# Kernel tuning notes

Measured on AMD Instinct MI355X. Metric: run time of the kernel, lower is better.

Reference implementation:

```python
import jax, jax.numpy as jnp
import numpy as np

EPS = 1e-6

def _log_g(x):
    # log of continuous g(x) = where(x>=0, x+0.5, sigmoid(x)) from minGRU paper
    return jnp.where(x >= 0, jnp.log(jax.nn.relu(x) + 0.5), -jax.nn.softplus(-x))

def setup_inputs() -> dict:
    key = jax.random.key(0)
    ks = jax.random.split(key, 4)
    B, S, D, E = 4, 2048, 1024, 8
    scale = D ** -0.5
    return {
        "inputs": jax.random.normal(ks[0], (B, S, D), dtype=jnp.float32),
        "norm_weight": jnp.ones((D,), jnp.float32),
        "router_w": jax.random.normal(ks[1], (E, D), jnp.float32) * scale,
        "router_b": jnp.zeros((E,), jnp.float32),
        "w_hg": jax.random.normal(ks[2], (E, 2 * D, D), jnp.float32) * scale,
        "w_out": jax.random.normal(ks[3], (E, D, D), jnp.float32) * scale,
    }

def reference(inputs, norm_weight, router_w, router_b, w_hg, w_out):
    D = inputs.shape[-1]
    # --- RMSNorm ---
    x = inputs * jax.lax.rsqrt(jnp.mean(inputs * inputs, axis=-1, keepdims=True) + EPS) * norm_weight
    # --- SMEAR: per-sample soft merge of expert weights via mean-pooled routing ---
    probs = jax.nn.softmax(jnp.mean(x, axis=1) @ router_w.T + router_b, axis=-1)  # [B,E]
    W_hg = jnp.einsum('be,ekd->bkd', probs, w_hg)    # [B,2D,D] merged to_hidden_and_gate
    W_out = jnp.einsum('be,eod->bod', probs, w_out)  # [B,D,D]  merged to_out
    # --- minGRU with merged weights (log-space parallel scan, no initial state) ---
    hg = jnp.einsum('bsd,bkd->bsk', x, W_hg)         # [B,S,2D]
    hidden, gate = hg[..., :D], hg[..., D:]
    log_coeffs = -jax.nn.softplus(gate)                      # log(1 - z_t)
    log_values = -jax.nn.softplus(-gate) + _log_g(hidden)    # log z_t + log g(h~_t)
    a_star = jnp.cumsum(log_coeffs, axis=1)
    log_h = a_star + jax.lax.cumlogsumexp(log_values - a_star, axis=1)
    h = jnp.exp(log_h)                               # [B,S,D] recurrent states
    new_state = h[:, -1:]                            # [B,1,D]
    out = jnp.einsum('bsk,bok->bso', h, W_out)       # proj_out
    aux_loss = jnp.zeros((), inputs.dtype)
    return (out + inputs, new_state, aux_loss)
```

## Files before the change

kernel.cpp:

```cpp
#include <hip/hip_runtime.h>
#include <hip/hip_bf16.h>

#define B_  4
#define S_  2048
#define D_  1024
#define E_  8
#define K2_ 2048

#define CHUNKS 32
#define CLEN   64

typedef __attribute__((ext_vector_type(8))) short short8;
typedef __attribute__((ext_vector_type(4))) float floatx4;

__device__ __forceinline__ void gld16(const void* g, const void* l) {
    __builtin_amdgcn_global_load_lds(
        (const __attribute__((address_space(1))) unsigned int*)g,
        (__attribute__((address_space(3))) unsigned int*)l, 16, 0, 0);
}

__global__ void rmsnorm_k(const float* __restrict__ in, const float* __restrict__ nw,
                          __hip_bfloat16* __restrict__ x) {
    int b = blockIdx.y, s = blockIdx.x, t = threadIdx.x;
    const float* row = in + ((size_t)b * S_ + s) * D_;
    float v[4]; float ss = 0.0f;
#pragma unroll
    for (int i = 0; i < 4; i++) { v[i] = row[t + 256 * i]; ss += v[i] * v[i]; }
#pragma unroll
    for (int o = 32; o > 0; o >>= 1) ss += __shfl_down(ss, o, 64);
    __shared__ float ls[4];
    if ((t & 63) == 0) ls[t >> 6] = ss;
    __syncthreads();
    float tot = ls[0] + ls[1] + ls[2] + ls[3];
    float rs = rsqrtf(tot * (1.0f / (float)D_) + 1e-6f);
    __hip_bfloat16* xr = x + ((size_t)b * S_ + s) * D_;
#pragma unroll
    for (int i = 0; i < 4; i++)
        xr[t + 256 * i] = __float2bfloat16(v[i] * rs * nw[t + 256 * i]);
}

__global__ void xsum_k(const __hip_bfloat16* __restrict__ x, float* __restrict__ xs) {
    int d = blockIdx.x * 256 + threadIdx.x;
    int b = blockIdx.y;
    int s0 = blockIdx.z * 128;
    const __hip_bfloat16* p = x + ((size_t)b * S_ + s0) * D_ + d;
    float acc = 0.0f;
#pragma unroll 4
    for (int s = 0; s < 128; s++) { acc += __bfloat162float(*p); p += D_; }
    atomicAdd(&xs[b * D_ + d], acc);
}

__global__ void router_k(const float* __restrict__ xs, const float* __restrict__ rw,
                         const float* __restrict__ rb, float* __restrict__ probs) {
    int t = threadIdx.x;
    int pair = t >> 3, sub = t & 7;
    int b = pair >> 3, e = pair & 7;
    float acc = 0.0f;
    for (int d = sub; d < D_; d += 8) acc += xs[b * D_ + d] * rw[e * D_ + d];
#pragma unroll
    for (int o = 4; o > 0; o >>= 1) acc += __shfl_down(acc, o, 8);
    __shared__ float lg[32];
    if (sub == 0) lg[pair] = acc * (1.0f / (float)S_) + rb[e];
    __syncthreads();
    if (t < 4) {
        float m = -1e30f;
        for (int e2 = 0; e2 < 8; e2++) m = fmaxf(m, lg[t * 8 + e2]);
        float ssum = 0.0f; float ex[8];
        for (int e2 = 0; e2 < 8; e2++) { ex[e2] = expf(lg[t * 8 + e2] - m); ssum += ex[e2]; }
        for (int e2 = 0; e2 < 8; e2++) probs[t * 8 + e2] = ex[e2] / ssum;
    }
}

__global__ void mix_k(const float* __restrict__ probs, const float* __restrict__ whg_e,
                      const float* __restrict__ wout_e, __hip_bfloat16* __restrict__ Whg,
                      __hip_bfloat16* __restrict__ Wout) {
    __shared__ float P[32];
    int t = threadIdx.x;
    if (t < 32) P[t] = probs[t];
    __syncthreads();
    size_t i = (size_t)blockIdx.x * 256 + t;
    const size_t T1 = (size_t)K2_ * D_;
    const size_t T2 = (size_t)D_ * D_;
    if (i < T1) {
        float a0 = 0, a1 = 0, a2 = 0, a3 = 0;
#pragma unroll
        for (int e = 0; e < 8; e++) {
            float w = whg_e[(size_t)e * T1 + i];
            a0 += P[0 * 8 + e] * w; a1 += P[1 * 8 + e] * w;
            a2 += P[2 * 8 + e] * w; a3 += P[3 * 8 + e] * w;
        }
        Whg[0 * T1 + i] = __float2bfloat16(a0); Whg[1 * T1 + i] = __float2bfloat16(a1);
        Whg[2 * T1 + i] = __float2bfloat16(a2); Whg[3 * T1 + i] = __float2bfloat16(a3);
    } else {
        size_t j = i - T1;
        float a0 = 0, a1 = 0, a2 = 0, a3 = 0;
#pragma unroll
        for (int e = 0; e < 8; e++) {
            float w = wout_e[(size_t)e * T2 + j];
            a0 += P[0 * 8 + e] * w; a1 += P[1 * 8 + e] * w;
            a2 += P[2 * 8 + e] * w; a3 += P[3 * 8 + e] * w;
        }
        Wout[0 * T2 + j] = __float2bfloat16(a0); Wout[1 * T2 + j] = __float2bfloat16(a1);
        Wout[2 * T2 + j] = __float2bfloat16(a2); Wout[3 * T2 + j] = __float2bfloat16(a3);
    }
}

__global__ __launch_bounds__(256) void gemm_hg_cv(
    const __hip_bfloat16* __restrict__ A, const __hip_bfloat16* __restrict__ Bm,
    float* __restrict__ cv) {
    const int K = D_;
    int bz = blockIdx.z;
    A  += (size_t)bz * S_ * D_;
    Bm += (size_t)bz * K2_ * D_;
    float2* CV = (float2*)cv + (size_t)bz * S_ * D_;
    int m0 = blockIdx.y * 128, n0 = blockIdx.x * 64;
    __shared__ __hip_bfloat16 lA[128][64];
    __shared__ __hip_bfloat16 lBh[64][64];
    __shared__ __hip_bfloat16 lBg[64][64];
    int t = threadIdx.x;
    int w = t >> 6, lane = t & 63;
    int lm = lane & 15, quad = lane >> 4;
    int wr = w >> 1, wc = w & 1;
    floatx4 acch[4][2] = {};
    floatx4 accg[4][2] = {};
    int srow = lane >> 3;
    int scolb = (lane & 7) * 16;
    const __hip_bfloat16* Bh = Bm;
    const __hip_bfloat16* Bg = Bm + (size_t)D_ * K;

    for (int k0 = 0; k0 < K; k0 += 64) {
#pragma unroll
        for (int it = 0; it < 4; it++) {
            int r0 = (w * 4 + it) * 8;
            gld16((const char*)(A + (size_t)(m0 + r0 + srow) * K + k0) + scolb,
                  &lA[r0][0]);
        }
#pragma unroll
        for (int it = 0; it < 2; it++) {
            int r0 = (w * 2 + it) * 8;
            gld16((const char*)(Bh + (size_t)(n0 + r0 + srow) * K + k0) + scolb,
                  &lBh[r0][0]);
            gld16((const char*)(Bg + (size_t)(n0 + r0 + srow) * K + k0) + scolb,
                  &lBg[r0][0]);
        }
        __syncthreads();
#pragma unroll
        for (int kk = 0; kk < 64; kk += 32) {
            short8 af[4], bh[2], bg[2];
#pragma unroll
            for (int i = 0; i < 4; i++)
                af[i] = *(const short8*)(&lA[wr * 64 + i * 16 + lm][kk + quad * 8]);
#pragma unroll
            for (int j = 0; j < 2; j++) {
                bh[j] = *(const short8*)(&lBh[wc * 32 + j * 16 + lm][kk + quad * 8]);
                bg[j] = *(const short8*)(&lBg[wc * 32 + j * 16 + lm][kk + quad * 8]);
            }
#pragma unroll
            for (int i = 0; i < 4; i++)
#pragma unroll
                for (int j = 0; j < 2; j++) {
                    acch[i][j] = __builtin_amdgcn_mfma_f32_16x16x32_bf16(
                        af[i], bh[j], acch[i][j], 0, 0, 0);
                    accg[i][j] = __builtin_amdgcn_mfma_f32_16x16x32_bf16(
                        af[i], bg[j], accg[i][j], 0, 0, 0);
                }
        }
        __syncthreads();
    }
#pragma unroll
    for (int i = 0; i < 4; i++) {
#pragma unroll
        for (int j = 0; j < 2; j++) {
#pragma unroll
            for (int r = 0; r < 4; r++) {
                int m = m0 + wr * 64 + i * 16 + quad * 4 + r;
                int n = n0 + wc * 32 + j * 16 + lm;
                float hid = acch[i][j][r];
                float g   = accg[i][j][r];
                float c  = 1.0f / (1.0f + expf(g));
                float sg = 1.0f / (1.0f + expf(-g));
                float gfn = (hid >= 0.0f) ? (hid + 0.5f)
                                          : (1.0f / (1.0f + expf(-hid)));
                CV[(size_t)m * D_ + n] = make_float2(c, sg * gfn);
            }
        }
    }
}

#define TM 128
#define TN 128
#define TBK 64
__global__ __launch_bounds__(256) void gemm_bf16_bt(
    const __hip_bfloat16* __restrict__ A, const __hip_bfloat16* __restrict__ Bm,
    float* __restrict__ C, const float* __restrict__ R,
    int M, int N, int K, size_t sa, size_t sb, size_t sc, size_t sr) {
    int bz = blockIdx.z;
    A += (size_t)bz * sa; Bm += (size_t)bz * sb; C += (size_t)bz * sc;
    if (R) R += (size_t)bz * sr;
    int m0 = blockIdx.y * TM, n0 = blockIdx.x * TN;
    __shared__ __hip_bfloat16 lA[TM][TBK];
    __shared__ __hip_bfloat16 lB[TN][TBK];
    int t = threadIdx.x;
    int w = t >> 6, lane = t & 63;
    int lm = lane & 15, quad = lane >> 4;
    int wr = w >> 1, wc = w & 1;
    floatx4 acc[4][4] = {};
    int srow = lane >> 3;
    int scolb = (lane & 7) * 16;

    for (int k0 = 0; k0 < K; k0 += TBK) {
#pragma unroll
        for (int it = 0; it < 4; it++) {
            int r0 = (w * 4 + it) * 8;
            gld16((const char*)(A + (size_t)(m0 + r0 + srow) * K + k0) + scolb,
                  &lA[r0][0]);
            gld16((const char*)(Bm + (size_t)(n0 + r0 + srow) * K + k0) + scolb,
                  &lB[r0][0]);
        }
        __syncthreads();
#pragma unroll
        for (int kk = 0; kk < TBK; kk += 32) {
            short8 af[4], bf[4];
#pragma unroll
            for (int i = 0; i < 4; i++)
                af[i] = *(const short8*)(&lA[wr * 64 + i * 16 + lm][kk + quad * 8]);
#pragma unroll
            for (int j = 0; j < 4; j++)
                bf[j] = *(const short8*)(&lB[wc * 64 + j * 16 + lm][kk + quad * 8]);
#pragma unroll
            for (int i = 0; i < 4; i++)
#pragma unroll
                for (int j = 0; j < 4; j++)
                    acc[i][j] = __builtin_amdgcn_mfma_f32_16x16x32_bf16(
                        af[i], bf[j], acc[i][j], 0, 0, 0);
        }
        __syncthreads();
    }
#pragma unroll
    for (int i = 0; i < 4; i++) {
#pragma unroll
        for (int j = 0; j < 4; j++) {
#pragma unroll
            for (int r = 0; r < 4; r++) {
                int m = m0 + wr * 64 + i * 16 + quad * 4 + r;
                int n = n0 + wc * 64 + j * 16 + lm;
                float v = acc[i][j][r];
                if (R) v += R[(size_t)m * N + n];
                C[(size_t)m * N + n] = v;
            }
        }
    }
}

__global__ void scanA_k(const float* __restrict__ cv, float* __restrict__ Cc,
                        float* __restrict__ Vc) {
    int b = blockIdx.z, c = blockIdx.y;
    int d = blockIdx.x * 256 + threadIdx.x;
    const float2* p = (const float2*)cv + ((size_t)b * S_ + c * CLEN) * D_ + d;
    float P = 1.0f, V = 0.0f;
    for (int s = 0; s < CLEN; s++) {
        float2 e = *p;
        P *= e.x;
        V = e.x * V + e.y;
        p += D_;
    }
    size_t idx = ((size_t)(b * CHUNKS + c)) * D_ + d;
    Cc[idx] = P; Vc[idx] = V;
}

__global__ void scanB_k(const float* __restrict__ Cc, const float* __restrict__ Vc,
                        float* __restrict__ Hi) {
    int b = blockIdx.y;
    int d = blockIdx.x * 256 + threadIdx.x;
    float h = 0.0f;
    for (int c = 0; c < CHUNKS; c++) {
        size_t idx = ((size_t)(b * CHUNKS + c)) * D_ + d;
        Hi[idx] = h;
        h = Cc[idx] * h + Vc[idx];
    }
}

__global__ void scanC_k(const float* __restrict__ cv, const float* __restrict__ Hi,
                        __hip_bfloat16* __restrict__ hout, float* __restrict__ ns) {
    int b = blockIdx.z, c = blockIdx.y;
    int d = blockIdx.x * 256 + threadIdx.x;
    const float2* p = (const float2*)cv + ((size_t)b * S_ + c * CLEN) * D_ + d;
    float h = Hi[((size_t)(b * CHUNKS + c)) * D_ + d];
    for (int s = 0; s < CLEN; s++) {
        float2 e = *p;
        h = e.x * h + e.y;
        hout[((size_t)b * S_ + c * CLEN + s) * D_ + d] = __float2bfloat16(h);
        if (c * CLEN + s == S_ - 1) ns[b * D_ + d] = h;
        p += D_;
    }
}

__global__ void aux_k(float* o) { if (threadIdx.x == 0) o[0] = 0.0f; }

extern "C" void kernel_launch(void* const* d_in, const int* in_sizes, int n_in,
                              void* d_out_v, int out_size, void* d_ws, size_t ws_size,
                              hipStream_t stream) {
    const float* inputs = (const float*)d_in[0];
    const float* nw     = (const float*)d_in[1];
    const float* rw     = (const float*)d_in[2];
    const float* rb     = (const float*)d_in[3];
    const float* whg_e  = (const float*)d_in[4];
    const float* wout_e = (const float*)d_in[5];
    float* out = (float*)d_out_v;

    float* ws = (float*)d_ws;
    float*          cv      = ws;
    __hip_bfloat16* x_bf    = (__hip_bfloat16*)(ws + 16777216);
    __hip_bfloat16* h_bf    = (__hip_bfloat16*)(ws + 20971520);
    __hip_bfloat16* Whg_bf  = (__hip_bfloat16*)(ws + 25165824);
    __hip_bfloat16* Wout_bf = (__hip_bfloat16*)(ws + 29360128);
    float* xsum  = ws + 31457280;
    float* probs = ws + 31461376;
    float* Cc    = ws + 31461408;
    float* Vc    = ws + 31592480;
    float* Hi    = ws + 31723552;

    hipMemsetAsync(xsum, 0, (size_t)B_ * D_ * sizeof(float), stream);

    rmsnorm_k<<<dim3(S_, B_), 256, 0, stream>>>(inputs, nw, x_bf);
    xsum_k<<<dim3(D_ / 256, B_, 16), 256, 0, stream>>>(x_bf, xsum);
    router_k<<<1, 256, 0, stream>>>(xsum, rw, rb, probs);
    mix_k<<<12288, 256, 0, stream>>>(probs, whg_e, wout_e, Whg_bf, Wout_bf);

    gemm_hg_cv<<<dim3(D_ / 64, S_ / 128, B_), 256, 0, stream>>>(x_bf, Whg_bf, cv);

    scanA_k<<<dim3(D_ / 256, CHUNKS, B_), 256, 0, stream>>>(cv, Cc, Vc);
    scanB_k<<<dim3(D_ / 256, B_), 256, 0, stream>>>(Cc, Vc, Hi);
    scanC_k<<<dim3(D_ / 256, CHUNKS, B_), 256, 0, stream>>>(
        cv, Hi, h_bf, out + (size_t)B_ * S_ * D_);

    gemm_bf16_bt<<<dim3(D_ / TN, S_ / TM, B_), 256, 0, stream>>>(
        h_bf, Wout_bf, out, inputs, S_, D_, D_,
        (size_t)S_ * D_, (size_t)D_ * D_, (size_t)S_ * D_, (size_t)S_ * D_);

    aux_k<<<1, 64, 0, stream>>>(out + (size_t)B_ * S_ * D_ + (size_t)B_ * D_);
}
```

Measured before the change: 358.5 us.

## Swizzle GEMM LDS tiles, vectorize scan kernels, fold aux write into router

Both bf16 GEMMs now XOR-swizzle the 16-byte columns of their LDS tiles, both when loading from global memory and when reading MFMA fragments, to avoid LDS bank conflicts. The chunked scan kernels each handle two channels per thread with float4 loads and bfloat162 stores. The chunk count is doubled and chunk length halved for more parallelism, and scratch offsets are enlarged to fit. The separate aux-loss kernel launch is removed and its zero store moved into the router kernel, saving one launch at the cost of a serial scanB that is twice as long.

Result: faster. 345.9 us (-3.5%).

```diff
diff --git a/kernel.cpp b/kernel.cpp
--- a/kernel.cpp
+++ b/kernel.cpp
@@ -7,8 +7,8 @@
 #define E_  8
 #define K2_ 2048
 
-#define CHUNKS 32
-#define CLEN   64
+#define CHUNKS 64
+#define CLEN   32
 
 typedef __attribute__((ext_vector_type(8))) short short8;
 typedef __attribute__((ext_vector_type(4))) float floatx4;
@@ -51,8 +51,10 @@
 }
 
 __global__ void router_k(const float* __restrict__ xs, const float* __restrict__ rw,
-                         const float* __restrict__ rb, float* __restrict__ probs) {
+                         const float* __restrict__ rb, float* __restrict__ probs,
+                         float* __restrict__ aux) {
     int t = threadIdx.x;
+    if (t == 255) *aux = 0.0f;
     int pair = t >> 3, sub = t & 7;
     int b = pair >> 3, e = pair & 7;
     float acc = 0.0f;
@@ -124,7 +126,7 @@
     floatx4 acch[4][2] = {};
     floatx4 accg[4][2] = {};
     int srow = lane >> 3;
-    int scolb = (lane & 7) * 16;
+    int swzb = ((lane & 7) ^ srow) * 16;
     const __hip_bfloat16* Bh = Bm;
     const __hip_bfloat16* Bg = Bm + (size_t)D_ * K;
 
@@ -132,15 +134,15 @@
 #pragma unroll
         for (int it = 0; it < 4; it++) {
             int r0 = (w * 4 + it) * 8;
-            gld16((const char*)(A + (size_t)(m0 + r0 + srow) * K + k0) + scolb,
+            gld16((const char*)(A + (size_t)(m0 + r0 + srow) * K + k0) + swzb,
                   &lA[r0][0]);
         }
 #pragma unroll
         for (int it = 0; it < 2; it++) {
             int r0 = (w * 2 + it) * 8;
-            gld16((const char*)(Bh + (size_t)(n0 + r0 + srow) * K + k0) + scolb,
+            gld16((const char*)(Bh + (size_t)(n0 + r0 + srow) * K + k0) + swzb,
                   &lBh[r0][0]);
-            gld16((const char*)(Bg + (size_t)(n0 + r0 + srow) * K + k0) + scolb,
+            gld16((const char*)(Bg + (size_t)(n0 + r0 + srow) * K + k0) + swzb,
                   &lBg[r0][0]);
         }
         __syncthreads();
@@ -148,12 +150,15 @@
         for (int kk = 0; kk < 64; kk += 32) {
             short8 af[4], bh[2], bg[2];
 #pragma unroll
-            for (int i = 0; i < 4; i++)
-                af[i] = *(const short8*)(&lA[wr * 64 + i * 16 + lm][kk + quad * 8]);
+            for (int i = 0; i < 4; i++) {
+                int p = (((kk >> 3) + quad) ^ (lm & 7)) * 8;
+                af[i] = *(const short8*)(&lA[wr * 64 + i * 16 + lm][p]);
+            }
 #pragma unroll
             for (int j = 0; j < 2; j++) {
-                bh[j] = *(const short8*)(&lBh[wc * 32 + j * 16 + lm][kk + quad * 8]);
-                bg[j] = *(const short8*)(&lBg[wc * 32 + j * 16 + lm][kk + quad * 8]);
+                int p = (((kk >> 3) + quad) ^ (lm & 7)) * 8;
+                bh[j] = *(const short8*)(&lBh[wc * 32 + j * 16 + lm][p]);
+                bg[j] = *(const short8*)(&lBg[wc * 32 + j * 16 + lm][p]);
             }
 #pragma unroll
             for (int i = 0; i < 4; i++)
@@ -206,15 +211,15 @@
     int wr = w >> 1, wc = w & 1;
     floatx4 acc[4][4] = {};
     int srow = lane >> 3;
-    int scolb = (lane & 7) * 16;
+    int swzb = ((lane & 7) ^ srow) * 16;
 
     for (int k0 = 0; k0 < K; k0 += TBK) {
 #pragma unroll
         for (int it = 0; it < 4; it++) {
             int r0 = (w * 4 + it) * 8;
-            gld16((const char*)(A + (size_t)(m0 + r0 + srow) * K + k0) + scolb,
+            gld16((const char*)(A + (size_t)(m0 + r0 + srow) * K + k0) + swzb,
                   &lA[r0][0]);
-            gld16((const char*)(Bm + (size_t)(n0 + r0 + srow) * K + k0) + scolb,
+            gld16((const char*)(Bm + (size_t)(n0 + r0 + srow) * K + k0) + swzb,
                   &lB[r0][0]);
         }
         __syncthreads();
@@ -222,11 +227,15 @@
         for (int kk = 0; kk < TBK; kk += 32) {
             short8 af[4], bf[4];
 #pragma unroll
-            for (int i = 0; i < 4; i++)
-                af[i] = *(const short8*)(&lA[wr * 64 + i * 16 + lm][kk + quad * 8]);
-#pragma unroll
-            for (int j = 0; j < 4; j++)
-                bf[j] = *(const short8*)(&lB[wc * 64 + j * 16 + lm][kk + quad * 8]);
+            for (int i = 0; i < 4; i++) {
+                int p = (((kk >> 3) + quad) ^ (lm & 7)) * 8;
+                af[i] = *(const short8*)(&lA[wr * 64 + i * 16 + lm][p]);
+            }
+#pragma unroll
+            for (int j = 0; j < 4; j++) {
+                int p = (((kk >> 3) + quad) ^ (lm & 7)) * 8;
+                bf[j] = *(const short8*)(&lB[wc * 64 + j * 16 + lm][p]);
+            }
 #pragma unroll
             for (int i = 0; i < 4; i++)
 #pragma unroll
@@ -255,17 +264,17 @@
 __global__ void scanA_k(const float* __restrict__ cv, float* __restrict__ Cc,
                         float* __restrict__ Vc) {
     int b = blockIdx.z, c = blockIdx.y;
-    int d = blockIdx.x * 256 + threadIdx.x;
-    const float2* p = (const float2*)cv + ((size_t)b * S_ + c * CLEN) * D_ + d;
-    float P = 1.0f, V = 0.0f;
+    int d2 = blockIdx.x * 256 + threadIdx.x;
+    const float4* p = (const float4*)cv + (size_t)(b * S_ + c * CLEN) * (D_ / 2) + d2;
+    float P0 = 1.0f, V0 = 0.0f, P1 = 1.0f, V1 = 0.0f;
+#pragma unroll 4
     for (int s = 0; s < CLEN; s++) {
-        float2 e = *p;
-        P *= e.x;
-        V = e.x * V + e.y;
-        p += D_;
-    }
-    size_t idx = ((size_t)(b * CHUNKS + c)) * D_ + d;
-    Cc[idx] = P; Vc[idx] = V;
+        float4 e = p[(size_t)s * (D_ / 2)];
+        P0 *= e.x; V0 = e.x * V0 + e.y;
+        P1 *= e.z; V1 = e.z * V1 + e.w;
+    }
+    size_t idx = ((size_t)(b * CHUNKS + c)) * D_ + 2 * d2;
+    Cc[idx] = P0; Vc[idx] = V0; Cc[idx + 1] = P1; Vc[idx + 1] = V1;
 }
 
 __global__ void scanB_k(const float* __restrict__ Cc, const float* __restrict__ Vc,
@@ -281,21 +290,23 @@
 }
 
 __global__ void scanC_k(const float* __restrict__ cv, const float* __restrict__ Hi,
-                        __hip_bfloat16* __restrict__ hout, float* __restrict__ ns) {
+                        __hip_bfloat162* __restrict__ hout, float* __restrict__ ns) {
     int b = blockIdx.z, c = blockIdx.y;
-    int d = blockIdx.x * 256 + threadIdx.x;
-    const float2* p = (const float2*)cv + ((size_t)b * S_ + c * CLEN) * D_ + d;
-    float h = Hi[((size_t)(b * CHUNKS + c)) * D_ + d];
+    int d2 = blockIdx.x * 256 + threadIdx.x;
+    const float4* p = (const float4*)cv + (size_t)(b * S_ + c * CLEN) * (D_ / 2) + d2;
+    size_t hidx = ((size_t)(b * CHUNKS + c)) * D_ + 2 * d2;
+    float h0 = Hi[hidx], h1 = Hi[hidx + 1];
+#pragma unroll 4
     for (int s = 0; s < CLEN; s++) {
-        float2 e = *p;
-        h = e.x * h + e.y;
-        hout[((size_t)b * S_ + c * CLEN + s) * D_ + d] = __float2bfloat16(h);
-        if (c * CLEN + s == S_ - 1) ns[b * D_ + d] = h;
-        p += D_;
-    }
-}
-
-__global__ void aux_k(float* o) { if (threadIdx.x == 0) o[0] = 0.0f; }
+        float4 e = p[(size_t)s * (D_ / 2)];
+        h0 = e.x * h0 + e.y;
+        h1 = e.z * h1 + e.w;
+        __hip_bfloat162 hh;
+        hh.x = __float2bfloat16(h0); hh.y = __float2bfloat16(h1);
+        hout[(size_t)(b * S_ + c * CLEN + s) * (D_ / 2) + d2] = hh;
+    }
+    if (c == CHUNKS - 1) { ns[b * D_ + 2 * d2] = h0; ns[b * D_ + 2 * d2 + 1] = h1; }
+}
 
 extern "C" void kernel_launch(void* const* d_in, const int* in_sizes, int n_in,
                               void* d_out_v, int out_size, void* d_ws, size_t ws_size,
@@ -317,26 +328,25 @@
     float* xsum  = ws + 31457280;
     float* probs = ws + 31461376;
     float* Cc    = ws + 31461408;
-    float* Vc    = ws + 31592480;
-    float* Hi    = ws + 31723552;
+    float* Vc    = ws + 31723552;
+    float* Hi    = ws + 31985696;
 
     hipMemsetAsync(xsum, 0, (size_t)B_ * D_ * sizeof(float), stream);
 
     rmsnorm_k<<<dim3(S_, B_), 256, 0, stream>>>(inputs, nw, x_bf);
     xsum_k<<<dim3(D_ / 256, B_, 16), 256, 0, stream>>>(x_bf, xsum);
-    router_k<<<1, 256, 0, stream>>>(xsum, rw, rb, probs);
+    router_k<<<1, 256, 0, stream>>>(xsum, rw, rb, probs,
+                                    out + (size_t)B_ * S_ * D_ + (size_t)B_ * D_);
     mix_k<<<12288, 256, 0, stream>>>(probs, whg_e, wout_e, Whg_bf, Wout_bf);
 
     gemm_hg_cv<<<dim3(D_ / 64, S_ / 128, B_), 256, 0, stream>>>(x_bf, Whg_bf, cv);
 
-    scanA_k<<<dim3(D_ / 256, CHUNKS, B_), 256, 0, stream>>>(cv, Cc, Vc);
+    scanA_k<<<dim3(D_ / 512, CHUNKS, B_), 256, 0, stream>>>(cv, Cc, Vc);
     scanB_k<<<dim3(D_ / 256, B_), 256, 0, stream>>>(Cc, Vc, Hi);
-    scanC_k<<<dim3(D_ / 256, CHUNKS, B_), 256, 0, stream>>>(
-        cv, Hi, h_bf, out + (size_t)B_ * S_ * D_);
+    scanC_k<<<dim3(D_ / 512, CHUNKS, B_), 256, 0, stream>>>(
+        cv, Hi, (__hip_bfloat162*)h_bf, out + (size_t)B_ * S_ * D_);
 
     gemm_bf16_bt<<<dim3(D_ / TN, S_ / TM, B_), 256, 0, stream>>>(
         h_bf, Wout_bf, out, inputs, S_, D_, D_,
         (size_t)S_ * D_, (size_t)D_ * D_, (size_t)S_ * D_, (size_t)S_ * D_);
-
-    aux_k<<<1, 64, 0, stream>>>(out + (size_t)B_ * S_ * D_ + (size_t)B_ * D_);
-}
+}
```
